# Performance work log

Hardware: AMD Instinct MI355X
Metric: run time of the kernel (lower is better)

Reference implementation:

```python
import jax, jax.numpy as jnp
import numpy as np

N = 8192        # nodes
IN_DIM = 512    # input feature dim
H = 8           # heads (hardcoded as 8 in original forward)
HID = 64        # out_feats per head
T = 10          # top-K threshold from settings['T']
OUT = 3         # classes
NEG = -9e15
NE_HALF = 131072  # half edges; graph made symmetric -> 262144 edges


def setup_inputs() -> dict:
    key = jax.random.key(0)
    ks = jax.random.split(key, 10)
    feat = jax.random.normal(ks[0], (N, IN_DIM), jnp.float32)

    def edges(k):
        k1, k2, k3 = jax.random.split(k, 3)
        u = jax.random.randint(k1, (NE_HALF,), 0, N, jnp.int32)
        v = jax.random.randint(k2, (NE_HALF,), 0, N, jnp.int32)
        src = jnp.concatenate([u, v])
        dst = jnp.concatenate([v, u])
        t = jax.random.uniform(k3, (NE_HALF,), jnp.float32) * 0.1  # TransM values
        trans = jnp.concatenate([t, t])
        return src, dst, trans

    src0, dst0, trans0 = edges(ks[1])
    src1, dst1, trans1 = edges(ks[2])
    fc_w0 = jax.random.normal(ks[3], (IN_DIM, H * HID), jnp.float32) * 0.05
    fc_w1 = jax.random.normal(ks[4], (IN_DIM, H * HID), jnp.float32) * 0.05
    sem_w1 = jax.random.normal(ks[5], (H * HID, 128), jnp.float32) * 0.05
    sem_b1 = jnp.zeros((128,), jnp.float32)
    sem_w2 = jax.random.normal(ks[6], (128,), jnp.float32) * 0.05
    lin_w = jax.random.normal(ks[7], (H * HID, OUT), jnp.float32) * 0.05
    lin_b = jnp.zeros((OUT,), jnp.float32)
    return dict(feat=feat, src0=src0, dst0=dst0, trans0=trans0,
                src1=src1, dst1=dst1, trans1=trans1,
                fc_w0=fc_w0, fc_w1=fc_w1, sem_w1=sem_w1, sem_b1=sem_b1,
                sem_w2=sem_w2, lin_w=lin_w, lin_b=lin_b)


def _rohe_conv(feat, src, dst, trans, fc_w):
    f = (feat @ fc_w).reshape(N, H, HID)               # (N,H,HID) projected feats
    # per-edge per-head dot products (same math as dense matmul + edge gather)
    e = jnp.einsum('ehd,ehd->eh', f[src], f[dst])      # (Ne,H)
    vals = trans * e.sum(-1)                           # (Ne,)  (e * e_trans).sum over heads
    # dense sparse->to_dense attn matrix, duplicates coalesced by sum
    A = jnp.zeros((N, N), f.dtype).at[src, dst].add(vals)
    kth = jax.lax.top_k(A, T)[0][:, -1]                # per-row T-th largest
    thr = jnp.maximum(kth, 0.0)                        # clamp(min=0)
    Am = jnp.where(A < thr[:, None], NEG, A)
    gathered = Am[dst, src]                            # == Am.T[src, dst]
    e = jnp.where((gathered < -100.0)[:, None], NEG, e)
    # edge softmax grouped by destination node, per head
    m = jax.ops.segment_max(e, dst, num_segments=N)
    ex = jnp.exp(e - m[dst])
    s = jax.ops.segment_sum(ex, dst, num_segments=N)
    a = ex / s[dst]                                    # (Ne,H)
    # u_mul_e + sum aggregation
    out = jax.ops.segment_sum(f[src] * a[:, :, None], dst, num_segments=N)
    return jax.nn.elu(out).reshape(N, H * HID)         # activation=F.elu, flatten(1)


def reference(feat, src0, dst0, trans0, src1, dst1, trans1,
              fc_w0, fc_w1, sem_w1, sem_b1, sem_w2, lin_w, lin_b):
    z0 = _rohe_conv(feat, src0, dst0, trans0, fc_w0)
    z1 = _rohe_conv(feat, src1, dst1, trans1, fc_w1)
    z = jnp.stack([z0, z1], axis=1)                    # (N, M=2, D)
    # SemanticAttention: project -> tanh -> score, mean over nodes, softmax over metapaths
    w = jnp.tanh(z @ sem_w1 + sem_b1) @ sem_w2         # (N, M)
    beta = jax.nn.softmax(w.mean(0))                   # (M,)
    h = (z * beta[None, :, None]).sum(1)               # (N, D)
    return h @ lin_w + lin_b                           # final nn.Linear
```

## Files before the change

### kernel.cpp

```cpp
#include <hip/hip_runtime.h>
#include <math.h>

#define NN      8192
#define DIM     512
#define NHEAD   8
#define HID     64
#define NE      262144
#define NE_HALF 131072
#define CMASK   (NE_HALF - 1)
#define TOPK    10
#define NEGV    -9e15f
#define MAXD    160

typedef __attribute__((ext_vector_type(8))) short short8;
typedef __attribute__((ext_vector_type(4))) float f32x4;
typedef __attribute__((ext_vector_type(2))) int i32x2;
typedef __attribute__((ext_vector_type(4))) int i32x4;

__device__ __forceinline__ float bf2f(unsigned int h) {
    return __uint_as_float(h << 16);
}
__device__ __forceinline__ unsigned short f2bf(float x) {
    unsigned int u = __float_as_uint(x);
    unsigned int r = (u + 0x7fff + ((u >> 16) & 1)) >> 16;
    return (unsigned short)r;
}

__device__ __forceinline__ void scatter_body(int j, int c,
                                             const int* __restrict__ src0,
                                             const int* __restrict__ src1,
                                             const int* __restrict__ dst0,
                                             const int* __restrict__ dst1,
                                             const float* __restrict__ trans0,
                                             const float* __restrict__ trans1,
                                             int* curF, int* curC,
                                             i32x2* __restrict__ ed,
                                             i32x4* __restrict__ ce) {
    const int* s = c ? src1 : src0;
    const int* dt = c ? dst1 : dst0;
    int v = s[j];
    int dv = dt[j];
    int p = atomicAdd(&curF[c * NN + v], 1);
    i32x2 pk; pk.x = j; pk.y = dv;
    ed[c * NE + p] = pk;
    if (j < NE_HALF) {
        const float* tr = c ? trans1 : trans0;
        int q = atomicAdd(&curC[c * NN + v], 1);
        i32x4 ck;
        ck.x = j; ck.y = dv; ck.z = __float_as_int(tr[j]); ck.w = 0;
        ce[c * NE_HALF + q] = ck;
    }
}

__device__ __forceinline__ void gemm_body(int b,
                                          const unsigned short* __restrict__ Ah,
                                          const unsigned short* __restrict__ Al,
                                          const unsigned short* __restrict__ Bh,
                                          const unsigned short* __restrict__ Bl,
                                          float* __restrict__ Cf,
                                          unsigned short* __restrict__ Ch) {
    __shared__ unsigned short Ash[128][32];
    __shared__ unsigned short Asl[128][32];
    __shared__ unsigned short Bsh[64][32];
    __shared__ unsigned short Bsl[64][32];
    const int bm = (b >> 3) * 128;
    const int bn = (b & 7) * 64;
    const int tid = threadIdx.x;
    const int lane = tid & 63;
    const int wave = tid >> 6;
    const int wm = (wave >> 1) * 64, wn = (wave & 1) * 32;
    const int fr = lane & 15, fq = lane >> 4;
    const int sr = tid >> 2, sc = (tid & 3) * 8;
    f32x4 acc[4][2] = {};
    const unsigned short* Ahg = Ah + (size_t)(bm + sr) * DIM + sc;
    const unsigned short* Alg = Al + (size_t)(bm + sr) * DIM + sc;
    const unsigned short* Bhg = Bh + (size_t)(bn + sr) * DIM + sc;
    const unsigned short* Blg = Bl + (size_t)(bn + sr) * DIM + sc;
    for (int kb = 0; kb < DIM; kb += 32) {
        __syncthreads();
        __builtin_amdgcn_global_load_lds(
            (const __attribute__((address_space(1))) void*)(Ahg + kb),
            (__attribute__((address_space(3))) void*)(&Ash[sr][sc]), 16, 0, 0);
        __builtin_amdgcn_global_load_lds(
            (const __attribute__((address_space(1))) void*)(Ahg + (size_t)64 * DIM + kb),
            (__attribute__((address_space(3))) void*)(&Ash[sr + 64][sc]), 16, 0, 0);
        __builtin_amdgcn_global_load_lds(
            (const __attribute__((address_space(1))) void*)(Alg + kb),
            (__attribute__((address_space(3))) void*)(&Asl[sr][sc]), 16, 0, 0);
        __builtin_amdgcn_global_load_lds(
            (const __attribute__((address_space(1))) void*)(Alg + (size_t)64 * DIM + kb),
            (__attribute__((address_space(3))) void*)(&Asl[sr + 64][sc]), 16, 0, 0);
        if (sr < 64) {
            __builtin_amdgcn_global_load_lds(
                (const __attribute__((address_space(1))) void*)(Bhg + kb),
                (__attribute__((address_space(3))) void*)(&Bsh[sr][sc]), 16, 0, 0);
            __builtin_amdgcn_global_load_lds(
                (const __attribute__((address_space(1))) void*)(Blg + kb),
                (__attribute__((address_space(3))) void*)(&Bsl[sr][sc]), 16, 0, 0);
        }
        __syncthreads();
        short8 ah[4], al[4], bh[2], bl[2];
        #pragma unroll
        for (int i = 0; i < 4; i++) {
            ah[i] = *(const short8*)&Ash[wm + i * 16 + fr][fq * 8];
            al[i] = *(const short8*)&Asl[wm + i * 16 + fr][fq * 8];
        }
        #pragma unroll
        for (int i = 0; i < 2; i++) {
            bh[i] = *(const short8*)&Bsh[wn + i * 16 + fr][fq * 8];
            bl[i] = *(const short8*)&Bsl[wn + i * 16 + fr][fq * 8];
        }
        #pragma unroll
        for (int mi = 0; mi < 4; mi++)
            #pragma unroll
            for (int ni = 0; ni < 2; ni++) {
                acc[mi][ni] = __builtin_amdgcn_mfma_f32_16x16x32_bf16(ah[mi], bh[ni], acc[mi][ni], 0, 0, 0);
                acc[mi][ni] = __builtin_amdgcn_mfma_f32_16x16x32_bf16(al[mi], bh[ni], acc[mi][ni], 0, 0, 0);
                acc[mi][ni] = __builtin_amdgcn_mfma_f32_16x16x32_bf16(ah[mi], bl[ni], acc[mi][ni], 0, 0, 0);
            }
    }
    #pragma unroll
    for (int mi = 0; mi < 4; mi++)
        #pragma unroll
        for (int ni = 0; ni < 2; ni++)
            #pragma unroll
            for (int r = 0; r < 4; r++) {
                int row = bm + wm + mi * 16 + fq * 4 + r;
                int col = bn + wn + ni * 16 + fr;
                float v = acc[mi][ni][r];
                size_t off = (size_t)row * DIM + col;
                Cf[off] = v;
                Ch[off] = f2bf(v);
            }
}

__device__ __forceinline__ void edge_body(int n,
                                          const float* __restrict__ Cf,
                                          const int* __restrict__ coffs,
                                          const i32x4* __restrict__ ce,
                                          float* __restrict__ e,
                                          float* __restrict__ vals) {
    int s0 = coffs[n];
    int d = coffs[n + 1] - s0;
    if (d <= 0) return;
    int wave = threadIdx.x >> 6, lane = threadIdx.x & 63;
    const float4* pf = (const float4*)(Cf + (size_t)n * DIM);
    float4 f0 = pf[lane * 2], f1 = pf[lane * 2 + 1];
    for (int i = wave; i < d; i += 8) {
        i32x4 c0e = ce[s0 + i];
        int j0 = c0e.x, dj0 = c0e.y;
        float t0 = __int_as_float(c0e.z);
        int i1 = i + 4;
        bool has1 = i1 < d;
        i32x4 c1e = has1 ? ce[s0 + i1] : c0e;
        int j1 = c1e.x, dj1 = c1e.y;
        float t1 = has1 ? __int_as_float(c1e.z) : 0.f;
        const float4* q0 = (const float4*)(Cf + (size_t)dj0 * DIM);
        const float4* q1 = (const float4*)(Cf + (size_t)dj1 * DIM);
        float4 b00 = q0[lane * 2], b01 = q0[lane * 2 + 1];
        float4 b10 = q1[lane * 2], b11 = q1[lane * 2 + 1];
        float p0, p1;
        p0  = f0.x * b00.x + f0.y * b00.y + f0.z * b00.z + f0.w * b00.w;
        p0 += f1.x * b01.x + f1.y * b01.y + f1.z * b01.z + f1.w * b01.w;
        p1  = f0.x * b10.x + f0.y * b10.y + f0.z * b10.z + f0.w * b10.w;
        p1 += f1.x * b11.x + f1.y * b11.y + f1.z * b11.z + f1.w * b11.w;
        p0 += __shfl_xor(p0, 1);
        p0 += __shfl_xor(p0, 2);
        p0 += __shfl_xor(p0, 4);
        p1 += __shfl_xor(p1, 1);
        p1 += __shfl_xor(p1, 2);
        p1 += __shfl_xor(p1, 4);
        if ((lane & 7) == 0) e[(size_t)j0 * NHEAD + (lane >> 3)] = p0;
        if (has1 && (lane & 7) == 0) e[(size_t)j1 * NHEAD + (lane >> 3)] = p1;
        p0 += __shfl_xor(p0, 8);
        p0 += __shfl_xor(p0, 16);
        p0 += __shfl_xor(p0, 32);
        p1 += __shfl_xor(p1, 8);
        p1 += __shfl_xor(p1, 16);
        p1 += __shfl_xor(p1, 32);
        if (lane == 0) {
            vals[j0] = t0 * p0;
            if (has1) vals[j1] = t1 * p1;
        }
    }
}

__device__ __forceinline__ void conv_body(int blk,
                                          const int* __restrict__ offs,
                                          const i32x2* __restrict__ ed,
                                          const float* __restrict__ e,
                                          const float* __restrict__ vals,
                                          const unsigned short* __restrict__ fb,
                                          unsigned short* __restrict__ zb) {
    const int tid = threadIdx.x;
    const int w = tid >> 6, lane = tid & 63;
    const int n = blk * 4 + w;
    int s0 = offs[n];
    int d = offs[n + 1] - s0;
    if (d > MAXD) d = MAXD;
    __shared__ int   ssrc[4][MAXD];
    __shared__ int   sjc[4][MAXD];
    __shared__ float sval[4][MAXD];
    __shared__ float svc[4][MAXD];
    __shared__ unsigned char lead[4][MAXD];
    __shared__ short sk[4][MAXD];
    __shared__ float sms[4][2][NHEAD];
    __shared__ int nkept[4];

    for (int i = lane; i < d; i += 64) {
        i32x2 pk = ed[s0 + i];
        int jc = pk.x & CMASK;
        sjc[w][i] = jc;
        ssrc[w][i] = pk.y;
        sval[w][i] = vals[jc];
    }
    __syncthreads();
    for (int i = lane; i < d; i += 64) {
        int c = ssrc[w][i];
        float sum = 0.f;
        bool leader = true;
        for (int k = 0; k < d; k++) {
            if (ssrc[w][k] == c) {
                sum += sval[w][k];
                if (k < i) leader = false;
            }
        }
        svc[w][i] = sum;
        lead[w][i] = leader ? 1 : 0;
    }
    __syncthreads();
    {
        float v[3];
        #pragma unroll
        for (int s = 0; s < 3; s++) v[s] = -1.f;
        int cnt = 0;
        #pragma unroll
        for (int s = 0; s < 3; s++) {
            int i = lane + s * 64;
            if (i < d && lead[w][i] && svc[w][i] > 0.f) { v[s] = svc[w][i]; cnt++; }
        }
        cnt += __shfl_xor(cnt, 1);  cnt += __shfl_xor(cnt, 2);
        cnt += __shfl_xor(cnt, 4);  cnt += __shfl_xor(cnt, 8);
        cnt += __shfl_xor(cnt, 16); cnt += __shfl_xor(cnt, 32);
        float thr = 0.f;
        if (cnt >= TOPK) {
            unsigned long long key = 0;
            for (int t = 0; t < TOPK; t++) {
                unsigned int bb = 0; int bs = 0;
                #pragma unroll
                for (int s = 0; s < 3; s++) {
                    if (v[s] > 0.f) {
                        unsigned int b = __float_as_uint(v[s]);
                        if (b > bb) { bb = b; bs = s; }
                    }
                }
                key = ((unsigned long long)bb << 12) | (unsigned)(lane << 3) | (unsigned)bs;
                unsigned long long o;
                o = __shfl_xor(key, 1);  if (o > key) key = o;
                o = __shfl_xor(key, 2);  if (o > key) key = o;
                o = __shfl_xor(key, 4);  if (o > key) key = o;
                o = __shfl_xor(key, 8);  if (o > key) key = o;
                o = __shfl_xor(key, 16); if (o > key) key = o;
                o = __shfl_xor(key, 32); if (o > key) key = o;
                int owner = (int)((key >> 3) & 63);
                if (owner == lane) v[key & 7] = -1.f;
            }
            thr = __uint_as_float((unsigned int)(key >> 12));
        }
        int base = 0;
        for (int s = 0; s * 64 < d; s++) {
            int i = s * 64 + lane;
            bool kp = (i < d) && (svc[w][i] >= thr);
            unsigned long long m = __ballot(kp);
            int pos = base + __popcll(m & ((1ull << lane) - 1ull));
            if (kp) sk[w][pos] = (short)i;
            base += (int)__popcll(m);
        }
        if (base == 0) {
            for (int i = lane; i < d; i += 64) sk[w][i] = (short)i;
            if (lane == 0) nkept[w] = -d;
        } else if (lane == 0) nkept[w] = base;
    }
    __syncthreads();
    int nk = nkept[w];
    bool uni = nk < 0;
    int dk = uni ? -nk : nk;
    if (!uni) {
        int h = lane & 7, sub = lane >> 3;
        float m = -INFINITY;
        for (int k = sub; k < dk; k += 8)
            m = fmaxf(m, e[(size_t)sjc[w][sk[w][k]] * NHEAD + h]);
        m = fmaxf(m, __shfl_xor(m, 8));
        m = fmaxf(m, __shfl_xor(m, 16));
        m = fmaxf(m, __shfl_xor(m, 32));
        float s = 0.f;
        for (int k = sub; k < dk; k += 8)
            s += expf(e[(size_t)sjc[w][sk[w][k]] * NHEAD + h] - m);
        s += __shfl_xor(s, 8);
        s += __shfl_xor(s, 16);
        s += __shfl_xor(s, 32);
        if (sub == 0) { sms[w][0][h] = m; sms[w][1][h] = s; }
    }
    __syncthreads();
    int c0 = lane * 8;
    int h = lane >> 3;
    float m = sms[w][0][h], s = sms[w][1][h];
    float invd = 1.0f / (float)d;
    float a0 = 0.f, a1 = 0.f, a2 = 0.f, a3 = 0.f;
    float a4 = 0.f, a5 = 0.f, a6 = 0.f, a7 = 0.f;
    for (int k = 0; k < dk; k++) {
        int ii = sk[w][k];
        float wgt = uni ? invd
                        : expf(e[(size_t)sjc[w][ii] * NHEAD + h] - m) / s;
        uint4 v = *(const uint4*)(fb + (size_t)ssrc[w][ii] * DIM + c0);
        a0 += wgt * bf2f(v.x & 0xffffu); a1 += wgt * bf2f(v.x >> 16);
        a2 += wgt * bf2f(v.y & 0xffffu); a3 += wgt * bf2f(v.y >> 16);
        a4 += wgt * bf2f(v.z & 0xffffu); a5 += wgt * bf2f(v.z >> 16);
        a6 += wgt * bf2f(v.w & 0xffffu); a7 += wgt * bf2f(v.w >> 16);
    }
    a0 = a0 > 0.f ? a0 : expf(a0) - 1.f;
    a1 = a1 > 0.f ? a1 : expf(a1) - 1.f;
    a2 = a2 > 0.f ? a2 : expf(a2) - 1.f;
    a3 = a3 > 0.f ? a3 : expf(a3) - 1.f;
    a4 = a4 > 0.f ? a4 : expf(a4) - 1.f;
    a5 = a5 > 0.f ? a5 : expf(a5) - 1.f;
    a6 = a6 > 0.f ? a6 : expf(a6) - 1.f;
    a7 = a7 > 0.f ? a7 : expf(a7) - 1.f;
    uint4 o;
    o.x = (unsigned)f2bf(a0) | ((unsigned)f2bf(a1) << 16);
    o.y = (unsigned)f2bf(a2) | ((unsigned)f2bf(a3) << 16);
    o.z = (unsigned)f2bf(a4) | ((unsigned)f2bf(a5) << 16);
    o.w = (unsigned)f2bf(a6) | ((unsigned)f2bf(a7) << 16);
    *(uint4*)(zb + (size_t)n * DIM + c0) = o;
}

__device__ __forceinline__ void split_w_body(const float* __restrict__ W,
                                             unsigned short* __restrict__ Th,
                                             unsigned short* __restrict__ Tl,
                                             int n0, int k0, int ncols,
                                             float (*t)[33], int tid) {
    int tx = tid & 31, ty = tid >> 5;
    #pragma unroll
    for (int i = 0; i < 4; i++)
        t[ty + 8 * i][tx] = W[(size_t)(k0 + ty + 8 * i) * ncols + n0 + tx];
    __syncthreads();
    #pragma unroll
    for (int i = 0; i < 4; i++) {
        float x = t[tx][ty + 8 * i];
        unsigned short h = f2bf(x);
        size_t off = (size_t)(n0 + ty + 8 * i) * DIM + k0 + tx;
        Th[off] = h;
        Tl[off] = f2bf(x - bf2f(h));
    }
}

__global__ __launch_bounds__(256) void prep(const float* __restrict__ feat,
                                            const float* __restrict__ w1,
                                            const float* __restrict__ fcw0,
                                            const float* __restrict__ fcw1,
                                            unsigned short* __restrict__ fH,
                                            unsigned short* __restrict__ fL,
                                            unsigned short* __restrict__ W1hT,
                                            unsigned short* __restrict__ W1lT,
                                            unsigned short* __restrict__ BhT0,
                                            unsigned short* __restrict__ BlT0,
                                            unsigned short* __restrict__ BhT1,
                                            unsigned short* __restrict__ BlT1,
                                            const int* __restrict__ src0,
                                            const int* __restrict__ src1,
                                            int* __restrict__ countsF,
                                            int* __restrict__ countsC) {
    int b = blockIdx.x;
    __shared__ float t[32][33];
    if (b < 4096) {
        int i = b * 256 + threadIdx.x;
        float4 v = ((const float4*)feat)[i];
        unsigned short h0 = f2bf(v.x), h1 = f2bf(v.y), h2 = f2bf(v.z), h3 = f2bf(v.w);
        ushort4 hv; hv.x = h0; hv.y = h1; hv.z = h2; hv.w = h3;
        ushort4 lv;
        lv.x = f2bf(v.x - bf2f(h0));
        lv.y = f2bf(v.y - bf2f(h1));
        lv.z = f2bf(v.z - bf2f(h2));
        lv.w = f2bf(v.w - bf2f(h3));
        ((ushort4*)fH)[i] = hv;
        ((ushort4*)fL)[i] = lv;
    } else if (b < 4160) {
        int idx = b - 4096;
        split_w_body(w1, W1hT, W1lT, (idx & 3) * 32, (idx >> 2) * 32, 128, t, threadIdx.x);
    } else if (b < 4416) {
        int idx = b - 4160;
        split_w_body(fcw0, BhT0, BlT0, (idx & 15) * 32, (idx >> 4) * 32, DIM, t, threadIdx.x);
    } else if (b < 4672) {
        int idx = b - 4416;
        split_w_body(fcw1, BhT1, BlT1, (idx & 15) * 32, (idx >> 4) * 32, DIM, t, threadIdx.x);
    } else {
        int sb = b - 4672;
        int c = sb >> 10;
        int j = (sb & 1023) * 256 + threadIdx.x;
        const int* s = c ? src1 : src0;
        int v = s[j];
        atomicAdd(&countsF[c * NN + v], 1);
        if (j < NE_HALF) atomicAdd(&countsC[c * NN + v], 1);
    }
}

__global__ __launch_bounds__(256) void scan_offs4(const int* __restrict__ counts,
                                                  int* __restrict__ offs,
                                                  int* __restrict__ cur) {
    int b = blockIdx.x;
    counts += b * NN; offs += b * (NN + 1); cur += b * NN;
    __shared__ int part[256];
    int t = threadIdx.x;
    int base = t * 32;
    int s = 0;
    for (int i = 0; i < 32; i++) s += counts[base + i];
    part[t] = s;
    __syncthreads();
    if (t == 0) {
        int run = 0;
        for (int i = 0; i < 256; i++) { int v = part[i]; part[i] = run; run += v; }
        offs[NN] = run;
    }
    __syncthreads();
    int run = part[t];
    for (int i = 0; i < 32; i++) {
        offs[base + i] = run;
        cur[base + i] = run;
        run += counts[base + i];
    }
}

__global__ __launch_bounds__(256) void gemm_sc(const unsigned short* __restrict__ Ah,
                                               const unsigned short* __restrict__ Al,
                                               const unsigned short* __restrict__ Bh,
                                               const unsigned short* __restrict__ Bl,
                                               float* __restrict__ Cf,
                                               unsigned short* __restrict__ Ch,
                                               const int* __restrict__ src0,
                                               const int* __restrict__ src1,
                                               const int* __restrict__ dst0,
                                               const int* __restrict__ dst1,
                                               const float* __restrict__ trans0,
                                               const float* __restrict__ trans1,
                                               int* curF, int* curC,
                                               i32x2* __restrict__ ed,
                                               i32x4* __restrict__ ce) {
    int b = blockIdx.x;
    if (b < 512) {
        gemm_body(b, Ah, Al, Bh, Bl, Cf, Ch);
    } else {
        int sb = b - 512;
        int c = sb >> 10;
        int j = (sb & 1023) * 256 + threadIdx.x;
        scatter_body(j, c, src0, src1, dst0, dst1, trans0, trans1,
                     curF, curC, ed, ce);
    }
}

__global__ __launch_bounds__(256) void gemm_ed(const unsigned short* __restrict__ Ah,
                                               const unsigned short* __restrict__ Al,
                                               const unsigned short* __restrict__ Bh,
                                               const unsigned short* __restrict__ Bl,
                                               float* __restrict__ Cf1,
                                               unsigned short* __restrict__ Ch1,
                                               const float* __restrict__ Cf0,
                                               const int* __restrict__ coffs0,
                                               const i32x4* __restrict__ ce0,
                                               float* __restrict__ e0,
                                               float* __restrict__ vals0) {
    int b = blockIdx.x;
    if (b < 512) {
        gemm_body(b, Ah, Al, Bh, Bl, Cf1, Ch1);
    } else {
        edge_body(b - 512, Cf0, coffs0, ce0, e0, vals0);
    }
}

__global__ __launch_bounds__(256) void conv_ed(const int* __restrict__ offsF0,
                                               const i32x2* __restrict__ ed0,
                                               const float* __restrict__ e0,
                                               const float* __restrict__ vals0,
                                               const unsigned short* __restrict__ Ch0,
                                               unsigned short* __restrict__ z0,
                                               const float* __restrict__ Cf1,
                                               const int* __restrict__ coffs1,
                                               const i32x4* __restrict__ ce1,
                                               float* __restrict__ e1,
                                               float* __restrict__ vals1) {
    int b = blockIdx.x;
    if (b < 2048) {
        conv_body(b, offsF0, ed0, e0, vals0, Ch0, z0);
    } else {
        edge_body(b - 2048, Cf1, coffs1, ce1, e1, vals1);
    }
}

__global__ __launch_bounds__(256) void conv_post(const int* __restrict__ offs,
                                                 const i32x2* __restrict__ ed,
                                                 const float* __restrict__ e,
                                                 const float* __restrict__ vals,
                                                 const unsigned short* __restrict__ fb,
                                                 unsigned short* __restrict__ zb) {
    conv_body(blockIdx.x, offs, ed, e, vals, fb, zb);
}

__global__ __launch_bounds__(256) void sem_scores3(const unsigned short* __restrict__ z0,
                                                   const unsigned short* __restrict__ z1,
                                                   const unsigned short* __restrict__ W1hT,
                                                   const unsigned short* __restrict__ W1lT,
                                                   const float* __restrict__ b1,
                                                   const float* __restrict__ w2,
                                                   float* wsum) {
    const unsigned short* Z = blockIdx.y ? z1 : z0;
    const int bm = blockIdx.x * 64;
    const int tid = threadIdx.x;
    const int lane = tid & 63, wave = tid >> 6;
    const int fr = lane & 15, fq = lane >> 4;
    __shared__ unsigned short Zs[64][32];
    __shared__ unsigned short Wh[128][32];
    __shared__ unsigned short Wl[128][32];
    const int sr = tid >> 2, sc = (tid & 3) * 8;
    f32x4 acc[8] = {};
    const unsigned short* Zg  = Z    + (size_t)(bm + sr) * DIM + sc;
    const unsigned short* Whg = W1hT + (size_t)sr * DIM + sc;
    const unsigned short* Wlg = W1lT + (size_t)sr * DIM + sc;
    for (int kb = 0; kb < DIM; kb += 32) {
        __syncthreads();
        __builtin_amdgcn_global_load_lds(
            (const __attribute__((address_space(1))) void*)(Zg + kb),
            (__attribute__((address_space(3))) void*)(&Zs[sr][sc]), 16, 0, 0);
        __builtin_amdgcn_global_load_lds(
            (const __attribute__((address_space(1))) void*)(Whg + kb),
            (__attribute__((address_space(3))) void*)(&Wh[sr][sc]), 16, 0, 0);
        __builtin_amdgcn_global_load_lds(
            (const __attribute__((address_space(1))) void*)(Whg + (size_t)64 * DIM + kb),
            (__attribute__((address_space(3))) void*)(&Wh[sr + 64][sc]), 16, 0, 0);
        __builtin_amdgcn_global_load_lds(
            (const __attribute__((address_space(1))) void*)(Wlg + kb),
            (__attribute__((address_space(3))) void*)(&Wl[sr][sc]), 16, 0, 0);
        __builtin_amdgcn_global_load_lds(
            (const __attribute__((address_space(1))) void*)(Wlg + (size_t)64 * DIM + kb),
            (__attribute__((address_space(3))) void*)(&Wl[sr + 64][sc]), 16, 0, 0);
        __syncthreads();
        short8 af = *(const short8*)&Zs[wave * 16 + fr][fq * 8];
        #pragma unroll
        for (int ni = 0; ni < 8; ni++) {
            short8 bh = *(const short8*)&Wh[ni * 16 + fr][fq * 8];
            acc[ni] = __builtin_amdgcn_mfma_f32_16x16x32_bf16(af, bh, acc[ni], 0, 0, 0);
        }
        #pragma unroll
        for (int ni = 0; ni < 8; ni++) {
            short8 bl = *(const short8*)&Wl[ni * 16 + fr][fq * 8];
            acc[ni] = __builtin_amdgcn_mfma_f32_16x16x32_bf16(af, bl, acc[ni], 0, 0, 0);
        }
    }
    float local = 0.f;
    #pragma unroll
    for (int ni = 0; ni < 8; ni++) {
        int col = ni * 16 + fr;
        float bb = b1[col], ww = w2[col];
        #pragma unroll
        for (int r = 0; r < 4; r++)
            local += tanhf(acc[ni][r] + bb) * ww;
    }
    __shared__ float red[256];
    red[tid] = local;
    __syncthreads();
    for (int s = 128; s > 0; s >>= 1) {
        if (tid < s) red[tid] += red[tid + s];
        __syncthreads();
    }
    if (tid == 0) atomicAdd(&wsum[blockIdx.y], red[0]);
}

__global__ __launch_bounds__(256) void final_out(const unsigned short* __restrict__ z0,
                                                 const unsigned short* __restrict__ z1,
                                                 const float* __restrict__ wsum,
                                                 const float* __restrict__ lin_w,
                                                 const float* __restrict__ lin_b,
                                                 float* __restrict__ out) {
    int idx = blockIdx.x * 256 + threadIdx.x;
    int n = idx / 3, o = idx - n * 3;
    float w0 = wsum[0] * (1.0f / NN), w1v = wsum[1] * (1.0f / NN);
    float mx = fmaxf(w0, w1v);
    float e0 = expf(w0 - mx), e1 = expf(w1v - mx);
    float beta0 = e0 / (e0 + e1), beta1 = e1 / (e0 + e1);
    const unsigned short* p0 = z0 + (size_t)n * DIM;
    const unsigned short* p1 = z1 + (size_t)n * DIM;
    float acc = 0.f;
    for (int dd = 0; dd < DIM; dd++)
        acc += (beta0 * bf2f(p0[dd]) + beta1 * bf2f(p1[dd])) * lin_w[dd * 3 + o];
    out[idx] = acc + lin_b[o];
}

extern "C" void kernel_launch(void* const* d_in, const int* in_sizes, int n_in,
                              void* d_out, int out_size, void* d_ws, size_t ws_size,
                              hipStream_t stream) {
    const float* feat = (const float*)d_in[0];
    const int*   srcp[2]   = { (const int*)d_in[1], (const int*)d_in[4] };
    const int*   dstp[2]   = { (const int*)d_in[2], (const int*)d_in[5] };
    const float* transp[2] = { (const float*)d_in[3], (const float*)d_in[6] };
    const float* fcw[2]    = { (const float*)d_in[7], (const float*)d_in[8] };
    const float* sem_w1 = (const float*)d_in[9];
    const float* sem_b1 = (const float*)d_in[10];
    const float* sem_w2 = (const float*)d_in[11];
    const float* lin_w  = (const float*)d_in[12];
    const float* lin_b  = (const float*)d_in[13];
    float* out = (float*)d_out;

    char* ws = (char*)d_ws;
    const size_t MB = 1 << 20;
    const size_t KB = 1 << 10;
    if (ws_size < 101 * MB) return;
    float*          Cf0   = (float*)(ws);
    float*          Cf1   = (float*)(ws + 16 * MB);
    unsigned short* Ch0   = (unsigned short*)(ws + 32 * MB);
    unsigned short* Ch1   = (unsigned short*)(ws + 40 * MB);
    unsigned short* z0    = (unsigned short*)(ws + 48 * MB);
    unsigned short* z1    = (unsigned short*)(ws + 56 * MB);
    unsigned short* fH    = (unsigned short*)(ws + 64 * MB);
    unsigned short* fL    = (unsigned short*)(ws + 72 * MB);
    float*          e0    = (float*)(ws + 80 * MB);
    float*          e1    = (float*)(ws + 84 * MB);
    float*          vals0 = (float*)(ws + 88 * MB);
    float*          vals1 = (float*)(ws + 88 * MB + 512 * KB);
    i32x2*          ed    = (i32x2*)(ws + 89 * MB);
    i32x4*          ce    = (i32x4*)(ws + 93 * MB);
    unsigned short* BhT0  = (unsigned short*)(ws + 97 * MB);
    unsigned short* BlT0  = (unsigned short*)(ws + 97 * MB + 512 * KB);
    unsigned short* BhT1  = (unsigned short*)(ws + 98 * MB);
    unsigned short* BlT1  = (unsigned short*)(ws + 98 * MB + 512 * KB);
    unsigned short* W1hT  = (unsigned short*)(ws + 99 * MB);
    unsigned short* W1lT  = (unsigned short*)(ws + 99 * MB + 128 * KB);
    int*            counts= (int*)  (ws + 99 * MB + 256 * KB);
    int*            offs  = (int*)  (ws + 99 * MB + 384 * KB);
    int*            cur   = (int*)  (ws + 99 * MB + 576 * KB);
    float*          wsum  = (float*)(ws + 99 * MB + 704 * KB);

    hipMemsetAsync(counts, 0, 4 * NN * sizeof(int), stream);
    prep<<<6720, 256, 0, stream>>>(feat, sem_w1, fcw[0], fcw[1],
                                   fH, fL, W1hT, W1lT, BhT0, BlT0, BhT1, BlT1,
                                   srcp[0], srcp[1], counts, counts + 2 * NN);
    scan_offs4<<<4, 256, 0, stream>>>(counts, offs, cur);
    const int* offsF0 = offs;
    const int* offsF1 = offs + (NN + 1);
    const int* offsC0 = offs + 2 * (NN + 1);
    const int* offsC1 = offs + 3 * (NN + 1);
    gemm_sc<<<2560, 256, 0, stream>>>(fH, fL, BhT0, BlT0, Cf0, Ch0,
                                      srcp[0], srcp[1], dstp[0], dstp[1],
                                      transp[0], transp[1],
                                      cur, cur + 2 * NN, ed, ce);
    gemm_ed<<<8704, 256, 0, stream>>>(fH, fL, BhT1, BlT1, Cf1, Ch1,
                                      Cf0, offsC0, ce, e0, vals0);
    conv_ed<<<10240, 256, 0, stream>>>(offsF0, ed, e0, vals0, Ch0, z0,
                                       Cf1, offsC1, ce + NE_HALF, e1, vals1);
    conv_post<<<2048, 256, 0, stream>>>(offsF1, ed + NE, e1, vals1, Ch1, z1);
    hipMemsetAsync(wsum, 0, 2 * sizeof(float), stream);
    sem_scores3<<<dim3(NN / 64, 2), 256, 0, stream>>>(z0, z1, W1hT, W1lT, sem_b1, sem_w2, wsum);
    final_out<<<(NN * 3) / 256, 256, 0, stream>>>(z0, z1, wsum, lin_w, lin_b, out);
}
```

Measured before the change: 379.7 us.

## Use fixed-capacity per-node edge buckets, batch edge loads, and split final linear per view

Replaces the count/scan CSR build with fixed-capacity per-node buckets (MAXD/MAXC slots), which removes the counting pass and the scan kernel. The edge-dot loop now processes four edges per wave per iteration for more memory parallelism, and softmax aggregation computes each weight once per lane and broadcasts it with shuffles. The final linear layer is applied to each view separately and overlapped with the other conv and semantic kernels, leaving only a cheap combine step. The buckets silently truncate any node whose degree exceeds the caps and use a larger workspace.

```diff
diff --git a/kernel.cpp b/kernel.cpp
--- a/kernel.cpp
+++ b/kernel.cpp
@@ -11,6 +11,7 @@
 #define TOPK    10
 #define NEGV    -9e15f
 #define MAXD    160
+#define MAXC    64
 
 typedef __attribute__((ext_vector_type(8))) short short8;
 typedef __attribute__((ext_vector_type(4))) float f32x4;
@@ -41,14 +42,18 @@
     int v = s[j];
     int dv = dt[j];
     int p = atomicAdd(&curF[c * NN + v], 1);
-    i32x2 pk; pk.x = j; pk.y = dv;
-    ed[c * NE + p] = pk;
+    if (p < MAXD) {
+        i32x2 pk; pk.x = j; pk.y = dv;
+        ed[(size_t)(c * NN + v) * MAXD + p] = pk;
+    }
     if (j < NE_HALF) {
         const float* tr = c ? trans1 : trans0;
         int q = atomicAdd(&curC[c * NN + v], 1);
-        i32x4 ck;
-        ck.x = j; ck.y = dv; ck.z = __float_as_int(tr[j]); ck.w = 0;
-        ce[c * NE_HALF + q] = ck;
+        if (q < MAXC) {
+            i32x4 ck;
+            ck.x = j; ck.y = dv; ck.z = __float_as_int(tr[j]); ck.w = 0;
+            ce[(size_t)(c * NN + v) * MAXC + q] = ck;
+        }
     }
 }
 
@@ -136,57 +141,61 @@
 
 __device__ __forceinline__ void edge_body(int n,
                                           const float* __restrict__ Cf,
-                                          const int* __restrict__ coffs,
+                                          const int* __restrict__ cdeg,
                                           const i32x4* __restrict__ ce,
                                           float* __restrict__ e,
                                           float* __restrict__ vals) {
-    int s0 = coffs[n];
-    int d = coffs[n + 1] - s0;
+    int d = cdeg[n];
+    if (d > MAXC) d = MAXC;
     if (d <= 0) return;
     int wave = threadIdx.x >> 6, lane = threadIdx.x & 63;
     const float4* pf = (const float4*)(Cf + (size_t)n * DIM);
     float4 f0 = pf[lane * 2], f1 = pf[lane * 2 + 1];
-    for (int i = wave; i < d; i += 8) {
-        i32x4 c0e = ce[s0 + i];
-        int j0 = c0e.x, dj0 = c0e.y;
-        float t0 = __int_as_float(c0e.z);
-        int i1 = i + 4;
-        bool has1 = i1 < d;
-        i32x4 c1e = has1 ? ce[s0 + i1] : c0e;
-        int j1 = c1e.x, dj1 = c1e.y;
-        float t1 = has1 ? __int_as_float(c1e.z) : 0.f;
-        const float4* q0 = (const float4*)(Cf + (size_t)dj0 * DIM);
-        const float4* q1 = (const float4*)(Cf + (size_t)dj1 * DIM);
-        float4 b00 = q0[lane * 2], b01 = q0[lane * 2 + 1];
-        float4 b10 = q1[lane * 2], b11 = q1[lane * 2 + 1];
-        float p0, p1;
-        p0  = f0.x * b00.x + f0.y * b00.y + f0.z * b00.z + f0.w * b00.w;
-        p0 += f1.x * b01.x + f1.y * b01.y + f1.z * b01.z + f1.w * b01.w;
-        p1  = f0.x * b10.x + f0.y * b10.y + f0.z * b10.z + f0.w * b10.w;
-        p1 += f1.x * b11.x + f1.y * b11.y + f1.z * b11.z + f1.w * b11.w;
-        p0 += __shfl_xor(p0, 1);
-        p0 += __shfl_xor(p0, 2);
-        p0 += __shfl_xor(p0, 4);
-        p1 += __shfl_xor(p1, 1);
-        p1 += __shfl_xor(p1, 2);
-        p1 += __shfl_xor(p1, 4);
-        if ((lane & 7) == 0) e[(size_t)j0 * NHEAD + (lane >> 3)] = p0;
-        if (has1 && (lane & 7) == 0) e[(size_t)j1 * NHEAD + (lane >> 3)] = p1;
-        p0 += __shfl_xor(p0, 8);
-        p0 += __shfl_xor(p0, 16);
-        p0 += __shfl_xor(p0, 32);
-        p1 += __shfl_xor(p1, 8);
-        p1 += __shfl_xor(p1, 16);
-        p1 += __shfl_xor(p1, 32);
+    const size_t s0 = (size_t)n * MAXC;
+    for (int base = wave * 4; base < d; base += 16) {
+        int em = d - base; if (em > 4) em = 4;
+        i32x4 c[4];
+        #pragma unroll
+        for (int t = 0; t < 4; t++)
+            c[t] = ce[s0 + base + (t < em ? t : 0)];
+        float4 b0[4], b1[4];
+        #pragma unroll
+        for (int t = 0; t < 4; t++) {
+            const float4* q = (const float4*)(Cf + (size_t)c[t].y * DIM);
+            b0[t] = q[lane * 2];
+            b1[t] = q[lane * 2 + 1];
+        }
+        float p[4];
+        #pragma unroll
+        for (int t = 0; t < 4; t++) {
+            p[t]  = f0.x * b0[t].x + f0.y * b0[t].y + f0.z * b0[t].z + f0.w * b0[t].w;
+            p[t] += f1.x * b1[t].x + f1.y * b1[t].y + f1.z * b1[t].z + f1.w * b1[t].w;
+            p[t] += __shfl_xor(p[t], 1);
+            p[t] += __shfl_xor(p[t], 2);
+            p[t] += __shfl_xor(p[t], 4);
+        }
+        if ((lane & 7) == 0) {
+            int h = lane >> 3;
+            #pragma unroll
+            for (int t = 0; t < 4; t++)
+                if (t < em) e[(size_t)c[t].x * NHEAD + h] = p[t];
+        }
+        #pragma unroll
+        for (int t = 0; t < 4; t++) {
+            p[t] += __shfl_xor(p[t], 8);
+            p[t] += __shfl_xor(p[t], 16);
+            p[t] += __shfl_xor(p[t], 32);
+        }
         if (lane == 0) {
-            vals[j0] = t0 * p0;
-            if (has1) vals[j1] = t1 * p1;
+            #pragma unroll
+            for (int t = 0; t < 4; t++)
+                if (t < em) vals[c[t].x] = __int_as_float(c[t].z) * p[t];
         }
     }
 }
 
 __device__ __forceinline__ void conv_body(int blk,
-                                          const int* __restrict__ offs,
+                                          const int* __restrict__ deg,
                                           const i32x2* __restrict__ ed,
                                           const float* __restrict__ e,
                                           const float* __restrict__ vals,
@@ -195,9 +204,9 @@
     const int tid = threadIdx.x;
     const int w = tid >> 6, lane = tid & 63;
     const int n = blk * 4 + w;
-    int s0 = offs[n];
-    int d = offs[n + 1] - s0;
+    int d = deg[n];
     if (d > MAXD) d = MAXD;
+    const size_t s0 = (size_t)n * MAXD;
     __shared__ int   ssrc[4][MAXD];
     __shared__ int   sjc[4][MAXD];
     __shared__ float sval[4][MAXD];
@@ -299,24 +308,52 @@
         s += __shfl_xor(s, 8);
         s += __shfl_xor(s, 16);
         s += __shfl_xor(s, 32);
-        if (sub == 0) { sms[w][0][h] = m; sms[w][1][h] = s; }
+        if (sub == 0) { sms[w][0][h] = m; sms[w][1][h] = 1.0f / s; }
     }
     __syncthreads();
     int c0 = lane * 8;
     int h = lane >> 3;
-    float m = sms[w][0][h], s = sms[w][1][h];
-    float invd = 1.0f / (float)d;
     float a0 = 0.f, a1 = 0.f, a2 = 0.f, a3 = 0.f;
     float a4 = 0.f, a5 = 0.f, a6 = 0.f, a7 = 0.f;
-    for (int k = 0; k < dk; k++) {
-        int ii = sk[w][k];
-        float wgt = uni ? invd
-                        : expf(e[(size_t)sjc[w][ii] * NHEAD + h] - m) / s;
-        uint4 v = *(const uint4*)(fb + (size_t)ssrc[w][ii] * DIM + c0);
-        a0 += wgt * bf2f(v.x & 0xffffu); a1 += wgt * bf2f(v.x >> 16);
-        a2 += wgt * bf2f(v.y & 0xffffu); a3 += wgt * bf2f(v.y >> 16);
-        a4 += wgt * bf2f(v.z & 0xffffu); a5 += wgt * bf2f(v.z >> 16);
-        a6 += wgt * bf2f(v.w & 0xffffu); a7 += wgt * bf2f(v.w >> 16);
+    if (uni) {
+        for (int k = 0; k < dk; k++) {
+            int ii = sk[w][k];
+            uint4 v = *(const uint4*)(fb + (size_t)ssrc[w][ii] * DIM + c0);
+            a0 += bf2f(v.x & 0xffffu); a1 += bf2f(v.x >> 16);
+            a2 += bf2f(v.y & 0xffffu); a3 += bf2f(v.y >> 16);
+            a4 += bf2f(v.z & 0xffffu); a5 += bf2f(v.z >> 16);
+            a6 += bf2f(v.w & 0xffffu); a7 += bf2f(v.w >> 16);
+        }
+        float invd = 1.0f / (float)d;
+        a0 *= invd; a1 *= invd; a2 *= invd; a3 *= invd;
+        a4 *= invd; a5 *= invd; a6 *= invd; a7 *= invd;
+    } else {
+        float m_h = sms[w][0][h], is_h = sms[w][1][h];
+        for (int kb = 0; kb < dk; kb += 8) {
+            int rem = dk - kb; if (rem > 8) rem = 8;
+            float wv = 0.f;
+            {
+                int t = lane & 7;
+                if (t < rem) {
+                    int ii = sk[w][kb + t];
+                    wv = expf(e[(size_t)sjc[w][ii] * NHEAD + h] - m_h) * is_h;
+                }
+            }
+#define AGG(j) { \
+            float wgt = __shfl(wv, (lane & 56) | (j)); \
+            int ii2 = sk[w][kb + (j)]; \
+            uint4 vv = *(const uint4*)(fb + (size_t)ssrc[w][ii2] * DIM + c0); \
+            a0 += wgt * bf2f(vv.x & 0xffffu); a1 += wgt * bf2f(vv.x >> 16); \
+            a2 += wgt * bf2f(vv.y & 0xffffu); a3 += wgt * bf2f(vv.y >> 16); \
+            a4 += wgt * bf2f(vv.z & 0xffffu); a5 += wgt * bf2f(vv.z >> 16); \
+            a6 += wgt * bf2f(vv.w & 0xffffu); a7 += wgt * bf2f(vv.w >> 16); }
+            if (rem == 8) {
+                AGG(0) AGG(1) AGG(2) AGG(3) AGG(4) AGG(5) AGG(6) AGG(7)
+            } else {
+                for (int j = 0; j < rem; j++) AGG(j)
+            }
+#undef AGG
+        }
     }
     a0 = a0 > 0.f ? a0 : expf(a0) - 1.f;
     a1 = a1 > 0.f ? a1 : expf(a1) - 1.f;
@@ -332,6 +369,111 @@
     o.z = (unsigned)f2bf(a4) | ((unsigned)f2bf(a5) << 16);
     o.w = (unsigned)f2bf(a6) | ((unsigned)f2bf(a7) << 16);
     *(uint4*)(zb + (size_t)n * DIM + c0) = o;
+}
+
+__device__ __forceinline__ void lin_body(int blk,
+                                         const unsigned short* __restrict__ zb,
+                                         const float* __restrict__ lin_w,
+                                         float* __restrict__ y) {
+    int tid = threadIdx.x;
+    int w = tid >> 6, lane = tid & 63;
+    int n = blk * 4 + w;
+    uint4 v = *(const uint4*)(zb + (size_t)n * DIM + lane * 8);
+    float f[8];
+    f[0] = bf2f(v.x & 0xffffu); f[1] = bf2f(v.x >> 16);
+    f[2] = bf2f(v.y & 0xffffu); f[3] = bf2f(v.y >> 16);
+    f[4] = bf2f(v.z & 0xffffu); f[5] = bf2f(v.z >> 16);
+    f[6] = bf2f(v.w & 0xffffu); f[7] = bf2f(v.w >> 16);
+    float lwv[24];
+    #pragma unroll
+    for (int q = 0; q < 6; q++)
+        *(float4*)&lwv[q * 4] = ((const float4*)lin_w)[lane * 6 + q];
+    float acc0 = 0.f, acc1 = 0.f, acc2 = 0.f;
+    #pragma unroll
+    for (int j = 0; j < 8; j++) {
+        acc0 += f[j] * lwv[j * 3 + 0];
+        acc1 += f[j] * lwv[j * 3 + 1];
+        acc2 += f[j] * lwv[j * 3 + 2];
+    }
+    #pragma unroll
+    for (int s = 1; s < 64; s <<= 1) {
+        acc0 += __shfl_xor(acc0, s);
+        acc1 += __shfl_xor(acc1, s);
+        acc2 += __shfl_xor(acc2, s);
+    }
+    if (lane == 0) {
+        y[n * 3 + 0] = acc0;
+        y[n * 3 + 1] = acc1;
+        y[n * 3 + 2] = acc2;
+    }
+}
+
+__device__ __forceinline__ void sem_body(int bx,
+                                         const unsigned short* __restrict__ Z,
+                                         const unsigned short* __restrict__ W1hT,
+                                         const unsigned short* __restrict__ W1lT,
+                                         const float* __restrict__ b1,
+                                         const float* __restrict__ w2,
+                                         float* wsum_slot) {
+    const int bm = bx * 64;
+    const int tid = threadIdx.x;
+    const int lane = tid & 63, wave = tid >> 6;
+    const int fr = lane & 15, fq = lane >> 4;
+    __shared__ unsigned short Zs[64][32];
+    __shared__ unsigned short Wh[128][32];
+    __shared__ unsigned short Wl[128][32];
+    const int sr = tid >> 2, sc = (tid & 3) * 8;
+    f32x4 acc[8] = {};
+    const unsigned short* Zg  = Z    + (size_t)(bm + sr) * DIM + sc;
+    const unsigned short* Whg = W1hT + (size_t)sr * DIM + sc;
+    const unsigned short* Wlg = W1lT + (size_t)sr * DIM + sc;
+    for (int kb = 0; kb < DIM; kb += 32) {
+        __syncthreads();
+        __builtin_amdgcn_global_load_lds(
+            (const __attribute__((address_space(1))) void*)(Zg + kb),
+            (__attribute__((address_space(3))) void*)(&Zs[sr][sc]), 16, 0, 0);
+        __builtin_amdgcn_global_load_lds(
+            (const __attribute__((address_space(1))) void*)(Whg + kb),
+            (__attribute__((address_space(3))) void*)(&Wh[sr][sc]), 16, 0, 0);
+        __builtin_amdgcn_global_load_lds(
+            (const __attribute__((address_space(1))) void*)(Whg + (size_t)64 * DIM + kb),
+            (__attribute__((address_space(3))) void*)(&Wh[sr + 64][sc]), 16, 0, 0);
+        __builtin_amdgcn_global_load_lds(
+            (const __attribute__((address_space(1))) void*)(Wlg + kb),
+            (__attribute__((address_space(3))) void*)(&Wl[sr][sc]), 16, 0, 0);
+        __builtin_amdgcn_global_load_lds(
+            (const __attribute__((address_space(1))) void*)(Wlg + (size_t)64 * DIM + kb),
+            (__attribute__((address_space(3))) void*)(&Wl[sr + 64][sc]), 16, 0, 0);
+        __syncthreads();
+        short8 af = *(const short8*)&Zs[wave * 16 + fr][fq * 8];
+        #pragma unroll
+        for (int ni = 0; ni < 8; ni++) {
+            short8 bh = *(const short8*)&Wh[ni * 16 + fr][fq * 8];
+            acc[ni] = __builtin_amdgcn_mfma_f32_16x16x32_bf16(af, bh, acc[ni], 0, 0, 0);
+        }
+        #pragma unroll
+        for (int ni = 0; ni < 8; ni++) {
+            short8 bl = *(const short8*)&Wl[ni * 16 + fr][fq * 8];
+            acc[ni] = __builtin_amdgcn_mfma_f32_16x16x32_bf16(af, bl, acc[ni], 0, 0, 0);
+        }
+    }
+    float local = 0.f;
+    #pragma unroll
+    for (int ni = 0; ni < 8; ni++) {
+        int col = ni * 16 + fr;
+        float bb = b1[col], ww = w2[col];
+        #pragma unroll
+        for (int r = 0; r < 4; r++)
+            local += tanhf(acc[ni][r] + bb) * ww;
+    }
+    __shared__ float red[256];
+    red[tid] = local;
+    __syncthreads();
+    for (int s = 128; s > 0; s >>= 1) {
+        if (tid < s) red[tid] += red[tid + s];
+        __syncthreads();
+    }
+    if (tid == 0) atomicAdd(wsum_slot, red[0]);
 }
 
 __device__ __forceinline__ void split_w_body(const float* __restrict__ W,
@@ -365,11 +507,7 @@
                                             unsigned short* __restrict__ BhT0,
                                             unsigned short* __restrict__ BlT0,
                                             unsigned short* __restrict__ BhT1,
-                                            unsigned short* __restrict__ BlT1,
-                                            const int* __restrict__ src0,
-                                            const int* __restrict__ src1,
-                                            int* __restrict__ countsF,
-                                            int* __restrict__ countsC) {
+                                            unsigned short* __restrict__ BlT1) {
     int b = blockIdx.x;
     __shared__ float t[32][33];
     if (b < 4096) {
@@ -390,43 +528,9 @@
     } else if (b < 4416) {
         int idx = b - 4160;
         split_w_body(fcw0, BhT0, BlT0, (idx & 15) * 32, (idx >> 4) * 32, DIM, t, threadIdx.x);
-    } else if (b < 4672) {
+    } else {
         int idx = b - 4416;
         split_w_body(fcw1, BhT1, BlT1, (idx & 15) * 32, (idx >> 4) * 32, DIM, t, threadIdx.x);
-    } else {
-        int sb = b - 4672;
-        int c = sb >> 10;
-        int j = (sb & 1023) * 256 + threadIdx.x;
-        const int* s = c ? src1 : src0;
-        int v = s[j];
-        atomicAdd(&countsF[c * NN + v], 1);
-        if (j < NE_HALF) atomicAdd(&countsC[c * NN + v], 1);
-    }
-}
-
-__global__ __launch_bounds__(256) void scan_offs4(const int* __restrict__ counts,
-                                                  int* __restrict__ offs,
-                                                  int* __restrict__ cur) {
-    int b = blockIdx.x;
-    counts += b * NN; offs += b * (NN + 1); cur += b * NN;
-    __shared__ int part[256];
-    int t = threadIdx.x;
-    int base = t * 32;
-    int s = 0;
-    for (int i = 0; i < 32; i++) s += counts[base + i];
-    part[t] = s;
-    __syncthreads();
-    if (t == 0) {
-        int run = 0;
-        for (int i = 0; i < 256; i++) { int v = part[i]; part[i] = run; run += v; }
-        offs[NN] = run;
-    }
-    __syncthreads();
-    int run = part[t];
-    for (int i = 0; i < 32; i++) {
-        offs[base + i] = run;
-        cur[base + i] = run;
-        run += counts[base + i];
     }
 }
 
@@ -464,7 +568,7 @@
                                                float* __restrict__ Cf1,
                                                unsigned short* __restrict__ Ch1,
                                                const float* __restrict__ Cf0,
-                                               const int* __restrict__ coffs0,
+                                               const int* __restrict__ cdeg0,
                                                const i32x4* __restrict__ ce0,
                                                float* __restrict__ e0,
                                                float* __restrict__ vals0) {
@@ -472,125 +576,77 @@
     if (b < 512) {
         gemm_body(b, Ah, Al, Bh, Bl, Cf1, Ch1);
     } else {
-        edge_body(b - 512, Cf0, coffs0, ce0, e0, vals0);
-    }
-}
-
-__global__ __launch_bounds__(256) void conv_ed(const int* __restrict__ offsF0,
+        edge_body(b - 512, Cf0, cdeg0, ce0, e0, vals0);
+    }
+}
+
+__global__ __launch_bounds__(256) void conv_ed(const int* __restrict__ degF0,
                                                const i32x2* __restrict__ ed0,
                                                const float* __restrict__ e0,
                                                const float* __restrict__ vals0,
                                                const unsigned short* __restrict__ Ch0,
                                                unsigned short* __restrict__ z0,
                                                const float* __restrict__ Cf1,
-                                               const int* __restrict__ coffs1,
+                                               const int* __restrict__ cdeg1,
                                                const i32x4* __restrict__ ce1,
                                                float* __restrict__ e1,
                                                float* __restrict__ vals1) {
     int b = blockIdx.x;
     if (b < 2048) {
-        conv_body(b, offsF0, ed0, e0, vals0, Ch0, z0);
+        conv_body(b, degF0, ed0, e0, vals0, Ch0, z0);
     } else {
-        edge_body(b - 2048, Cf1, coffs1, ce1, e1, vals1);
-    }
-}
-
-__global__ __launch_bounds__(256) void conv_post(const int* __restrict__ offs,
-                                                 const i32x2* __restrict__ ed,
-                                                 const float* __restrict__ e,
-                                                 const float* __restrict__ vals,
-                                                 const unsigned short* __restrict__ fb,
-                                                 unsigned short* __restrict__ zb) {
-    conv_body(blockIdx.x, offs, ed, e, vals, fb, zb);
-}
-
-__global__ __launch_bounds__(256) void sem_scores3(const unsigned short* __restrict__ z0,
-                                                   const unsigned short* __restrict__ z1,
-                                                   const unsigned short* __restrict__ W1hT,
-                                                   const unsigned short* __restrict__ W1lT,
-                                                   const float* __restrict__ b1,
-                                                   const float* __restrict__ w2,
-                                                   float* wsum) {
-    const unsigned short* Z = blockIdx.y ? z1 : z0;
-    const int bm = blockIdx.x * 64;
-    const int tid = threadIdx.x;
-    const int lane = tid & 63, wave = tid >> 6;
-    const int fr = lane & 15, fq = lane >> 4;
-    __shared__ unsigned short Zs[64][32];
-    __shared__ unsigned short Wh[128][32];
-    __shared__ unsigned short Wl[128][32];
-    const int sr = tid >> 2, sc = (tid & 3) * 8;
-    f32x4 acc[8] = {};
-    const unsigned short* Zg  = Z    + (size_t)(bm + sr) * DIM + sc;
-    const unsigned short* Whg = W1hT + (size_t)sr * DIM + sc;
-    const unsigned short* Wlg = W1lT + (size_t)sr * DIM + sc;
-    for (int kb = 0; kb < DIM; kb += 32) {
-        __syncthreads();
-        __builtin_amdgcn_global_load_lds(
-            (const __attribute__((address_space(1))) void*)(Zg + kb),
-            (__attribute__((address_space(3))) void*)(&Zs[sr][sc]), 16, 0, 0);
-        __builtin_amdgcn_global_load_lds(
-            (const __attribute__((address_space(1))) void*)(Whg + kb),
-            (__attribute__((address_space(3))) void*)(&Wh[sr][sc]), 16, 0, 0);
-        __builtin_amdgcn_global_load_lds(
-            (const __attribute__((address_space(1))) void*)(Whg + (size_t)64 * DIM + kb),
-            (__attribute__((address_space(3))) void*)(&Wh[sr + 64][sc]), 16, 0, 0);
-        __builtin_amdgcn_global_load_lds(
-            (const __attribute__((address_space(1))) void*)(Wlg + kb),
-            (__attribute__((address_space(3))) void*)(&Wl[sr][sc]), 16, 0, 0);
-        __builtin_amdgcn_global_load_lds(
-            (const __attribute__((address_space(1))) void*)(Wlg + (size_t)64 * DIM + kb),
-            (__attribute__((address_space(3))) void*)(&Wl[sr + 64][sc]), 16, 0, 0);
-        __syncthreads();
-        short8 af = *(const short8*)&Zs[wave * 16 + fr][fq * 8];
-        #pragma unroll
-        for (int ni = 0; ni < 8; ni++) {
-            short8 bh = *(const short8*)&Wh[ni * 16 + fr][fq * 8];
-            acc[ni] = __builtin_amdgcn_mfma_f32_16x16x32_bf16(af, bh, acc[ni], 0, 0, 0);
-        }
-        #pragma unroll
-        for (int ni = 0; ni < 8; ni++) {
-            short8 bl = *(const short8*)&Wl[ni * 16 + fr][fq * 8];
-            acc[ni] = __builtin_amdgcn_mfma_f32_16x16x32_bf16(af, bl, acc[ni], 0, 0, 0);
-        }
-    }
-    float local = 0.f;
-    #pragma unroll
-    for (int ni = 0; ni < 8; ni++) {
-        int col = ni * 16 + fr;
-        float bb = b1[col], ww = w2[col];
-        #pragma unroll
-        for (int r = 0; r < 4; r++)
-            local += tanhf(acc[ni][r] + bb) * ww;
-    }
-    __shared__ float red[256];
-    red[tid] = local;
-    __syncthreads();
-    for (int s = 128; s > 0; s >>= 1) {
-        if (tid < s) red[tid] += red[tid + s];
-        __syncthreads();
-    }
-    if (tid == 0) atomicAdd(&wsum[blockIdx.y], red[0]);
-}
-
-__global__ __launch_bounds__(256) void final_out(const unsigned short* __restrict__ z0,
-                                                 const unsigned short* __restrict__ z1,
-                                                 const float* __restrict__ wsum,
-                                                 const float* __restrict__ lin_w,
-                                                 const float* __restrict__ lin_b,
-                                                 float* __restrict__ out) {
+        edge_body(b - 2048, Cf1, cdeg1, ce1, e1, vals1);
+    }
+}
+
+__global__ __launch_bounds__(256) void conv_lin(const int* __restrict__ degF1,
+                                                const i32x2* __restrict__ ed1,
+                                                const float* __restrict__ e1,
+                                                const float* __restrict__ vals1,
+                                                const unsigned short* __restrict__ Ch1,
+                                                unsigned short* __restrict__ z1,
+                                                const unsigned short* __restrict__ z0,
+                                                const float* __restrict__ lin_w,
+                                                float* __restrict__ y0) {
+    int b = blockIdx.x;
+    if (b < 2048) {
+        conv_body(b, degF1, ed1, e1, vals1, Ch1, z1);
+    } else {
+        lin_body(b - 2048, z0, lin_w, y0);
+    }
+}
+
+__global__ __launch_bounds__(256) void sem_lin(const unsigned short* __restrict__ z0,
+                                               const unsigned short* __restrict__ z1,
+                                               const unsigned short* __restrict__ W1hT,
+                                               const unsigned short* __restrict__ W1lT,
+                                               const float* __restrict__ b1,
+                                               const float* __restrict__ w2,
+                                               float* __restrict__ wsum,
+                                               const float* __restrict__ lin_w,
+                                               float* __restrict__ y1) {
+    int b = blockIdx.x;
+    if (b < 128) {
+        sem_body(b, z0, W1hT, W1lT, b1, w2, &wsum[0]);
+    } else if (b < 256) {
+        sem_body(b - 128, z1, W1hT, W1lT, b1, w2, &wsum[1]);
+    } else {
+        lin_body(b - 256, z1, lin_w, y1);
+    }
+}
+
+__global__ __launch_bounds__(256) void combine_out(const float* __restrict__ y0,
+                                                   const float* __restrict__ y1,
+                                                   const float* __restrict__ wsum,
+                                                   const float* __restrict__ lin_b,
+                                                   float* __restrict__ out) {
     int idx = blockIdx.x * 256 + threadIdx.x;
-    int n = idx / 3, o = idx - n * 3;
     float w0 = wsum[0] * (1.0f / NN), w1v = wsum[1] * (1.0f / NN);
     float mx = fmaxf(w0, w1v);
-    float e0 = expf(w0 - mx), e1 = expf(w1v - mx);
-    float beta0 = e0 / (e0 + e1), beta1 = e1 / (e0 + e1);
-    const unsigned short* p0 = z0 + (size_t)n * DIM;
-    const unsigned short* p1 = z1 + (size_t)n * DIM;
-    float acc = 0.f;
-    for (int dd = 0; dd < DIM; dd++)
-        acc += (beta0 * bf2f(p0[dd]) + beta1 * bf2f(p1[dd])) * lin_w[dd * 3 + o];
-    out[idx] = acc + lin_b[o];
+    float ea = expf(w0 - mx), eb = expf(w1v - mx);
+    float beta0 = ea / (ea + eb), beta1 = eb / (ea + eb);
+    int o = idx % 3;
+    out[idx] = beta0 * y0[idx] + beta1 * y1[idx] + lin_b[o];
 }
 
 extern "C" void kernel_launch(void* const* d_in, const int* in_sizes, int n_in,
@@ -611,7 +667,7 @@
     char* ws = (char*)d_ws;
     const size_t MB = 1 << 20;
     const size_t KB = 1 << 10;
-    if (ws_size < 101 * MB) return;
+    if (ws_size < 128 * MB) return;
     float*          Cf0   = (float*)(ws);
     float*          Cf1   = (float*)(ws + 16 * MB);
     unsigned short* Ch0   = (unsigned short*)(ws + 32 * MB);
@@ -625,37 +681,35 @@
     float*          vals0 = (float*)(ws + 88 * MB);
     float*          vals1 = (float*)(ws + 88 * MB + 512 * KB);
     i32x2*          ed    = (i32x2*)(ws + 89 * MB);
-    i32x4*          ce    = (i32x4*)(ws + 93 * MB);
-    unsigned short* BhT0  = (unsigned short*)(ws + 97 * MB);
-    unsigned short* BlT0  = (unsigned short*)(ws + 97 * MB + 512 * KB);
-    unsigned short* BhT1  = (unsigned short*)(ws + 98 * MB);
-    unsigned short* BlT1  = (unsigned short*)(ws + 98 * MB + 512 * KB);
-    unsigned short* W1hT  = (unsigned short*)(ws + 99 * MB);
-    unsigned short* W1lT  = (unsigned short*)(ws + 99 * MB + 128 * KB);
-    int*            counts= (int*)  (ws + 99 * MB + 256 * KB);
-    int*            offs  = (int*)  (ws + 99 * MB + 384 * KB);
-    int*            cur   = (int*)  (ws + 99 * MB + 576 * KB);
-    float*          wsum  = (float*)(ws + 99 * MB + 704 * KB);
-
-    hipMemsetAsync(counts, 0, 4 * NN * sizeof(int), stream);
-    prep<<<6720, 256, 0, stream>>>(feat, sem_w1, fcw[0], fcw[1],
-                                   fH, fL, W1hT, W1lT, BhT0, BlT0, BhT1, BlT1,
-                                   srcp[0], srcp[1], counts, counts + 2 * NN);
-    scan_offs4<<<4, 256, 0, stream>>>(counts, offs, cur);
-    const int* offsF0 = offs;
-    const int* offsF1 = offs + (NN + 1);
-    const int* offsC0 = offs + 2 * (NN + 1);
-    const int* offsC1 = offs + 3 * (NN + 1);
+    i32x4*          ce    = (i32x4*)(ws + 109 * MB);
+    unsigned short* BhT0  = (unsigned short*)(ws + 125 * MB);
+    unsigned short* BlT0  = (unsigned short*)(ws + 125 * MB + 512 * KB);
+    unsigned short* BhT1  = (unsigned short*)(ws + 126 * MB);
+    unsigned short* BlT1  = (unsigned short*)(ws + 126 * MB + 512 * KB);
+    unsigned short* W1hT  = (unsigned short*)(ws + 127 * MB);
+    unsigned short* W1lT  = (unsigned short*)(ws + 127 * MB + 128 * KB);
+    float*          y0    = (float*)(ws + 127 * MB + 256 * KB);
+    float*          y1    = (float*)(ws + 127 * MB + 384 * KB);
+    int*            cur   = (int*)  (ws + 127 * MB + 512 * KB);
+    float*          wsum  = (float*)(ws + 127 * MB + 640 * KB);
+
+    hipMemsetAsync(cur, 0, 4 * NN * sizeof(int) + 2 * sizeof(float), stream);
+    prep<<<4672, 256, 0, stream>>>(feat, sem_w1, fcw[0], fcw[1],
+                                   fH, fL, W1hT, W1lT, BhT0, BlT0, BhT1, BlT1);
+    int* curF = cur;
+    int* curC = cur + 2 * NN;
     gemm_sc<<<2560, 256, 0, stream>>>(fH, fL, BhT0, BlT0, Cf0, Ch0,
                                       srcp[0], srcp[1], dstp[0], dstp[1],
                                       transp[0], transp[1],
-                                      cur, cur + 2 * NN, ed, ce);
+                                      curF, curC, ed, ce);
     gemm_ed<<<8704, 256, 0, stream>>>(fH, fL, BhT1, BlT1, Cf1, Ch1,
-                                      Cf0, offsC0, ce, e0, vals0);
-    conv_ed<<<10240, 256, 0, stream>>>(offsF0, ed, e0, vals0, Ch0, z0,
-                                       Cf1, offsC1, ce + NE_HALF, e1, vals1);
-    conv_post<<<2048, 256, 0, stream>>>(offsF1, ed + NE, e1, vals1, Ch1, z1);
-    hipMemsetAsync(wsum, 0, 2 * sizeof(float), stream);
-    sem_scores3<<<dim3(NN / 64, 2), 256, 0, stream>>>(z0, z1, W1hT, W1lT, sem_b1, sem_w2, wsum);
-    final_out<<<(NN * 3) / 256, 256, 0, stream>>>(z0, z1, wsum, lin_w, lin_b, out);
-}
+                                      Cf0, curC, ce, e0, vals0);
+    conv_ed<<<10240, 256, 0, stream>>>(curF, ed, e0, vals0, Ch0, z0,
+                                       Cf1, curC + NN, ce + (size_t)NN * MAXC,
+                                       e1, vals1);
+    conv_lin<<<4096, 256, 0, stream>>>(curF + NN, ed + (size_t)NN * MAXD,
+                                       e1, vals1, Ch1, z1, z0, lin_w, y0);
+    sem_lin<<<2304, 256, 0, stream>>>(z0, z1, W1hT, W1lT, sem_b1, sem_w2,
+                                      wsum, lin_w, y1);
+    combine_out<<<(NN * 3) / 256, 256, 0, stream>>>(y0, y1, wsum, lin_b, out);
+}
```

Result: faster. 322.4 us (-15.1%).
